# Kernel optimization log

Hardware: AMD Instinct MI355X
Metric: run time of the kernel (lower is better)

## Reference

```python
import jax, jax.numpy as jnp
import numpy as np

TEMPERATURE = 0.07
NEG = -1e9  # stand-in for -inf on the diagonal; exp(NEG) == 0


def setup_inputs() -> dict:
    key = jax.random.key(0)
    k1, k2, k3 = jax.random.split(key, 3)
    B, D = 4096, 1024
    return {
        "anchor_features": jax.random.normal(k1, (B, D), dtype=jnp.float32),
        "positive_features": jax.random.normal(k2, (B, D), dtype=jnp.float32),
        "labels": jax.random.randint(k3, (B,), 0, 2),
    }


def reference(anchor_features, positive_features, labels):
    B = anchor_features.shape[0]
    # L2-normalize (normalize=True)
    a = anchor_features / jnp.linalg.norm(anchor_features, axis=1, keepdims=True)
    p = positive_features / jnp.linalg.norm(positive_features, axis=1, keepdims=True)
    feats = jnp.concatenate([a, p], axis=0)                      # [2B, D]
    sim = jnp.matmul(feats, feats.T) / TEMPERATURE               # [2B, 2B]
    diag = jnp.eye(2 * B, dtype=bool)
    sim = jnp.where(diag, NEG, sim)                              # mask self-similarity
    # logsumexp over all non-self entries per row (diag contributes exp(NEG)=0)
    lse = jax.nn.logsumexp(sim, axis=1)                          # [2B]
    # positive pair similarity: sim[i, i+B] == sim[i+B, i] == <a_i, p_i>/t
    cross = jnp.sum(a * p, axis=1) / TEMPERATURE                 # [B]
    pos_sim = jnp.concatenate([cross, cross])                    # [2B]
    lab = jnp.concatenate([labels, labels]).astype(sim.dtype)    # [2B], 0/1
    per_row = (-pos_sim + lse) * lab
    num_pos = jnp.sum(lab)
    return jnp.where(num_pos > 0, jnp.sum(per_row) / num_pos, jnp.float32(0.0))
```

## Files before the change

### kernel.cpp

```cpp
#include <hip/hip_runtime.h>
#include <hip/hip_bf16.h>

#define TEMP_INV (1.0f / 0.07f)
#define LOG2E 1.4426950408889634f
#define LN2 0.6931471805599453f
#define CFIX 21.0f

typedef __attribute__((ext_vector_type(4))) float f32x4;

__device__ __forceinline__ void gload16(const unsigned char* g,
                                        unsigned char* l) {
  __builtin_amdgcn_global_load_lds(
      (const __attribute__((address_space(1))) void*)g,
      (__attribute__((address_space(3))) void*)l, 16, 0, 0);
}

__global__ __launch_bounds__(256) void norm_kernel(
    const float* __restrict__ A, const float* __restrict__ P,
    unsigned char* __restrict__ F, float* __restrict__ cross,
    float* __restrict__ lsum, int B, int D) {
  const int row = blockIdx.x;
  const int t = threadIdx.x;
  {
    const int zi = row * 256 + t;
    if (zi < 2 * B) lsum[zi] = 0.f;
  }
  const float4* a4 = reinterpret_cast<const float4*>(A + (size_t)row * D);
  const float4* p4 = reinterpret_cast<const float4*>(P + (size_t)row * D);
  const int n4 = D >> 2;
  float sa = 0.f, sp = 0.f, sx = 0.f;
  for (int i = t; i < n4; i += 256) {
    float4 av = a4[i], pv = p4[i];
    sa += av.x * av.x + av.y * av.y + av.z * av.z + av.w * av.w;
    sp += pv.x * pv.x + pv.y * pv.y + pv.z * pv.z + pv.w * pv.w;
    sx += av.x * pv.x + av.y * pv.y + av.z * pv.z + av.w * pv.w;
  }
#pragma unroll
  for (int off = 32; off; off >>= 1) {
    sa += __shfl_down(sa, off);
    sp += __shfl_down(sp, off);
    sx += __shfl_down(sx, off);
  }
  __shared__ float red[3][4];
  const int wid = t >> 6, lane = t & 63;
  if (lane == 0) { red[0][wid] = sa; red[1][wid] = sp; red[2][wid] = sx; }
  __syncthreads();
  sa = red[0][0] + red[0][1] + red[0][2] + red[0][3];
  sp = red[1][0] + red[1][1] + red[1][2] + red[1][3];
  sx = red[2][0] + red[2][1] + red[2][2] + red[2][3];
  const float ian = rsqrtf(sa), ipn = rsqrtf(sp);
  const float ia = ian * 16.f, ip = ipn * 16.f;
  unsigned char* fa = F + (size_t)row * D;
  unsigned char* fp = F + (size_t)(B + row) * D;
  for (int i = t; i < n4; i += 256) {
    float4 av = a4[i], pv = p4[i];
    int qa = 0, qp = 0;
    qa = __builtin_amdgcn_cvt_pk_fp8_f32(av.x * ia, av.y * ia, qa, false);
    qa = __builtin_amdgcn_cvt_pk_fp8_f32(av.z * ia, av.w * ia, qa, true);
    qp = __builtin_amdgcn_cvt_pk_fp8_f32(pv.x * ip, pv.y * ip, qp, false);
    qp = __builtin_amdgcn_cvt_pk_fp8_f32(pv.z * ip, pv.w * ip, qp, true);
    reinterpret_cast<int*>(fa)[i] = qa;
    reinterpret_cast<int*>(fp)[i] = qp;
  }
  if (t == 0) cross[row] = sx * ian * ipn;
}

#define VT 16

__global__ __launch_bounds__(512, 2) void gram_lse_kernel(
    const unsigned char* __restrict__ F, float* __restrict__ lsum, int NN,
    int D) {
  __shared__ unsigned char lds8[4][2][2][8192];
  const int nrb = NN >> 8;
  const int ntri = nrb * (nrb + 1) / 2;
  int b = blockIdx.x;
  b = (b & 7) * (gridDim.x >> 3) + (b >> 3);
  const int lin0 = b * 3;

  const int t = threadIdx.x;
  const int lane = t & 63, w = t >> 6;
  const int lo = lane & 15, hi = lane >> 4;
  const int wr = w >> 2, wn = w & 3;

  const int ci = t;
  const int lrS = ci >> 3, cuS = (ci & 7) ^ (lrS & 7);
  const int trowS = lrS * 4 + (cuS >> 1), kcS = (cuS & 1) << 4;
  const int dstW = w * 1024;

  int offA[8], offB[4];
#pragma unroll
  for (int mf = 0; mf < 8; ++mf) {
    const int r = wr * 128 + mf * 16 + lo;
    const int lr = r >> 2;
    const int cu = ((r & 3) << 1) | (hi >> 1);
    offA[mf] = lr * 128 + ((cu ^ (lr & 7)) << 4) + ((hi & 1) << 3);
  }
#pragma unroll
  for (int nf = 0; nf < 4; ++nf) {
    const int r = wn * 64 + nf * 16 + lo;
    const int lr = r >> 2;
    const int cu = ((r & 3) << 1) | (hi >> 1);
    offB[nf] = lr * 128 + ((cu ^ (lr & 7)) << 4) + ((hi & 1) << 3);
  }

  const float scl = LOG2E * TEMP_INV / 256.f;

  for (int ti = 0; ti < 3; ++ti) {
    const int lin = lin0 + ti;
    int by = (int)((sqrtf(8.f * (float)lin + 1.f) - 1.f) * 0.5f);
    while ((by + 1) * (by + 2) / 2 <= lin) ++by;
    while (by * (by + 1) / 2 > lin) --by;
    const int bx = lin - by * (by + 1) / 2;
    const int r0 = bx * 256;
    const int c0 = by * 256;
    const bool diag = (bx == by);

    const unsigned char* srcA = F + (size_t)(c0 + trowS) * D + kcS;
    const unsigned char* srcB = F + (size_t)(r0 + trowS) * D + kcS;

#define STAGE_A(T, KS)                                              \
  do {                                                              \
    int v_ = (T); if (v_ > VT - 1) v_ = VT - 1;                     \
    gload16(srcA + v_ * 64 + (KS) * 32, &lds8[(T) & 3][0][KS][dstW]); \
  } while (0)
#define STAGE_B(T, KS)                                              \
  do {                                                              \
    int v_ = (T); if (v_ > VT - 1) v_ = VT - 1;                     \
    gload16(srcB + v_ * 64 + (KS) * 32, &lds8[(T) & 3][1][KS][dstW]); \
  } while (0)

    f32x4 acc[8][4];
#pragma unroll
    for (int a = 0; a < 8; ++a)
#pragma unroll
      for (int bb = 0; bb < 4; ++bb) acc[a][bb] = (f32x4){0.f, 0.f, 0.f, 0.f};

#pragma unroll
    for (int pt = 0; pt < 3; ++pt) {
      STAGE_A(pt, 0); STAGE_B(pt, 0);
      STAGE_A(pt, 1); STAGE_B(pt, 1);
    }

    for (int v = 0; v < VT; ++v) {
      const int buf = v & 3;
      asm volatile("s_waitcnt vmcnt(8)" ::: "memory");
      __builtin_amdgcn_s_barrier();
      asm volatile("" ::: "memory");

#pragma unroll
      for (int KS = 0; KS < 2; ++KS) {
        const unsigned char* RA = &lds8[buf][0][KS][0];
        const unsigned char* RB = &lds8[buf][1][KS][0];
        long aF[8], bF[4];
#pragma unroll
        for (int nf = 0; nf < 4; ++nf) bF[nf] = *(const long*)(RB + offB[nf]);
#pragma unroll
        for (int mf = 0; mf < 8; ++mf) aF[mf] = *(const long*)(RA + offA[mf]);

        if (KS == 0) { STAGE_A(v + 3, 0); STAGE_B(v + 3, 0); }
        else         { STAGE_A(v + 3, 1); STAGE_B(v + 3, 1); }

        __builtin_amdgcn_s_setprio(1);
#pragma unroll
        for (int mf = 0; mf < 8; ++mf)
#pragma unroll
          for (int nf = 0; nf < 4; ++nf)
            acc[mf][nf] = __builtin_amdgcn_mfma_f32_16x16x32_fp8_fp8(
                aF[mf], bF[nf], acc[mf][nf], 0, 0, 0);
        __builtin_amdgcn_s_setprio(0);
      }
      asm volatile("" ::: "memory");
    }

    float s_i[4] = {0.f, 0.f, 0.f, 0.f};
    float s_j[32];
#pragma unroll
    for (int q = 0; q < 32; ++q) s_j[q] = 0.f;
    {
      const int jb2 = c0 + wr * 128;
#pragma unroll
      for (int nf = 0; nf < 4; ++nf) {
        const int dg = (r0 + wn * 64 + nf * 16 + lo) - jb2;
#pragma unroll
        for (int mf = 0; mf < 8; ++mf)
#pragma unroll
          for (int rg = 0; rg < 4; ++rg) {
            const int jloc = mf * 16 + hi * 4 + rg;
            float e = exp2f(acc[mf][nf][rg] * scl - CFIX);
            if (diag && dg == jloc) e = 0.f;
            s_i[nf] += e;
            s_j[mf * 4 + rg] += e;
          }
      }
    }
#pragma unroll
    for (int nf = 0; nf < 4; ++nf) {
      float v = s_i[nf];
      v += __shfl_xor(v, 16);
      v += __shfl_xor(v, 32);
      if (hi == 0) atomicAdd(&lsum[r0 + wn * 64 + nf * 16 + lo], v);
    }
    if (!diag) {
#pragma unroll
      for (int q = 0; q < 32; ++q) {
        float v = s_j[q];
        v += __shfl_xor(v, 1);
        v += __shfl_xor(v, 2);
        v += __shfl_xor(v, 4);
        v += __shfl_xor(v, 8);
        if (lo == 0)
          atomicAdd(&lsum[c0 + wr * 128 + (q >> 2) * 16 + hi * 4 + (q & 3)],
                    v);
      }
    }

    asm volatile("s_waitcnt vmcnt(0)" ::: "memory");
    __builtin_amdgcn_s_barrier();
    asm volatile("" ::: "memory");
#undef STAGE_A
#undef STAGE_B
  }
}

__global__ __launch_bounds__(256) void finalize_part(
    const float* __restrict__ lsum, const float* __restrict__ cross,
    const int* __restrict__ labels, float* __restrict__ bsum,
    float* __restrict__ bcnt, int B) {
  const int NN = 2 * B;
  const int i = blockIdx.x * 256 + threadIdx.x;
  float sum = 0.f, cnt = 0.f;
  if (i < NN) {
    const float lse = LN2 * (CFIX + log2f(lsum[i]));
    const float lab = (float)labels[i % B];
    sum = (lse - cross[i % B] * TEMP_INV) * lab;
    cnt = lab;
  }
#pragma unroll
  for (int off = 32; off; off >>= 1) {
    sum += __shfl_down(sum, off);
    cnt += __shfl_down(cnt, off);
  }
  __shared__ float rs[4], rc[4];
  const int wid = threadIdx.x >> 6, lane = threadIdx.x & 63;
  if (lane == 0) { rs[wid] = sum; rc[wid] = cnt; }
  __syncthreads();
  if (threadIdx.x == 0) {
    bsum[blockIdx.x] = rs[0] + rs[1] + rs[2] + rs[3];
    bcnt[blockIdx.x] = rc[0] + rc[1] + rc[2] + rc[3];
  }
}

__global__ __launch_bounds__(64) void finalize_final(
    const float* __restrict__ bsum, const float* __restrict__ bcnt,
    float* __restrict__ out, int nb) {
  const int t = threadIdx.x;
  float s = (t < nb) ? bsum[t] : 0.f;
  float c = (t < nb) ? bcnt[t] : 0.f;
#pragma unroll
  for (int off = 32; off; off >>= 1) {
    s += __shfl_down(s, off);
    c += __shfl_down(c, off);
  }
  if (t == 0) out[0] = (c > 0.f) ? s / c : 0.f;
}

extern "C" void kernel_launch(void* const* d_in, const int* in_sizes, int n_in,
                              void* d_out, int out_size, void* d_ws, size_t ws_size,
                              hipStream_t stream) {
  const float* A = (const float*)d_in[0];
  const float* P = (const float*)d_in[1];
  const int* labels = (const int*)d_in[2];
  float* out = (float*)d_out;
  const int B = in_sizes[2];
  const int D = in_sizes[0] / B;
  const int NN = 2 * B;

  char* ws = (char*)d_ws;
  unsigned char* F = (unsigned char*)ws;
  size_t off = (size_t)NN * D;
  off = (off + 255) & ~(size_t)255;
  float* cross = (float*)(ws + off);
  off += (size_t)B * sizeof(float);
  off = (off + 255) & ~(size_t)255;
  float* lsum = (float*)(ws + off);
  off += (size_t)NN * sizeof(float);
  off = (off + 255) & ~(size_t)255;
  float* bsum = (float*)(ws + off);
  off += 64 * sizeof(float);
  float* bcnt = (float*)(ws + off);

  norm_kernel<<<B, 256, 0, stream>>>(A, P, F, cross, lsum, B, D);
  const int nrb = NN >> 8;
  const int ntri = nrb * (nrb + 1) / 2;
  gram_lse_kernel<<<ntri / 3, 512, 0, stream>>>(F, lsum, NN, D);
  const int nb = (NN + 255) / 256;
  finalize_part<<<nb, 256, 0, stream>>>(lsum, cross, labels, bsum, bcnt, B);
  finalize_final<<<1, 64, 0, stream>>>(bsum, bcnt, out, nb);
}
```

Measured before the change: 115.4 us.

## Use 16x16x128 scaled FP8 MFMA with double-buffered 128-wide K staging, one tile per block

Replaces the 16x16x32 FP8 MFMA with the MX-scaled 16x16x128 f8f6f4 MFMA (unit scales), so each instruction covers four times the K depth. LDS staging changes from a 4-deep ring of 64-byte K slices to a 2-deep double buffer of 128-byte K slices, with a new swizzle and 128-bit LDS fragment reads. The grid now launches one block per triangle tile instead of each block looping over three tiles, which gives more blocks and less per-block serial work. The cost is a shallower pipeline that waits on vmcnt(0) every step, plus a higher register footprint for the 8-int fragments.

Measured after the change: 135.6 us. 17.6% more time.

```diff
diff --git a/kernel.cpp b/kernel.cpp
--- a/kernel.cpp
+++ b/kernel.cpp
@@ -7,6 +7,7 @@
 #define CFIX 21.0f
 
 typedef __attribute__((ext_vector_type(4))) float f32x4;
+typedef __attribute__((ext_vector_type(8))) int i32x8;
 
 __device__ __forceinline__ void gload16(const unsigned char* g,
                                         unsigned char* l) {
@@ -65,161 +66,147 @@
   if (t == 0) cross[row] = sx * ian * ipn;
 }
 
-#define VT 16
+#define UP 8
 
 __global__ __launch_bounds__(512, 2) void gram_lse_kernel(
     const unsigned char* __restrict__ F, float* __restrict__ lsum, int NN,
     int D) {
-  __shared__ unsigned char lds8[4][2][2][8192];
+  __shared__ unsigned char lds8[2][2][2][16384];
   const int nrb = NN >> 8;
   const int ntri = nrb * (nrb + 1) / 2;
-  int b = blockIdx.x;
-  b = (b & 7) * (gridDim.x >> 3) + (b >> 3);
-  const int lin0 = b * 3;
+  int lin = blockIdx.x;
+  lin = (lin & 7) * (ntri >> 3) + (lin >> 3);
+  int by = (int)((sqrtf(8.f * (float)lin + 1.f) - 1.f) * 0.5f);
+  while ((by + 1) * (by + 2) / 2 <= lin) ++by;
+  while (by * (by + 1) / 2 > lin) --by;
+  const int bx = lin - by * (by + 1) / 2;
+  const int r0 = bx * 256;
+  const int c0 = by * 256;
+  const bool diag = (bx == by);
 
   const int t = threadIdx.x;
   const int lane = t & 63, w = t >> 6;
   const int lo = lane & 15, hi = lane >> 4;
   const int wr = w >> 2, wn = w & 3;
 
-  const int ci = t;
-  const int lrS = ci >> 3, cuS = (ci & 7) ^ (lrS & 7);
-  const int trowS = lrS * 4 + (cuS >> 1), kcS = (cuS & 1) << 4;
-  const int dstW = w * 1024;
-
-  int offA[8], offB[4];
-#pragma unroll
-  for (int mf = 0; mf < 8; ++mf) {
-    const int r = wr * 128 + mf * 16 + lo;
-    const int lr = r >> 2;
-    const int cu = ((r & 3) << 1) | (hi >> 1);
-    offA[mf] = lr * 128 + ((cu ^ (lr & 7)) << 4) + ((hi & 1) << 3);
-  }
-#pragma unroll
-  for (int nf = 0; nf < 4; ++nf) {
-    const int r = wn * 64 + nf * 16 + lo;
-    const int lr = r >> 2;
-    const int cu = ((r & 3) << 1) | (hi >> 1);
-    offB[nf] = lr * 128 + ((cu ^ (lr & 7)) << 4) + ((hi & 1) << 3);
-  }
-
-  const float scl = LOG2E * TEMP_INV / 256.f;
-
-  for (int ti = 0; ti < 3; ++ti) {
-    const int lin = lin0 + ti;
-    int by = (int)((sqrtf(8.f * (float)lin + 1.f) - 1.f) * 0.5f);
-    while ((by + 1) * (by + 2) / 2 <= lin) ++by;
-    while (by * (by + 1) / 2 > lin) --by;
-    const int bx = lin - by * (by + 1) / 2;
-    const int r0 = bx * 256;
-    const int c0 = by * 256;
-    const bool diag = (bx == by);
-
-    const unsigned char* srcA = F + (size_t)(c0 + trowS) * D + kcS;
-    const unsigned char* srcB = F + (size_t)(r0 + trowS) * D + kcS;
-
-#define STAGE_A(T, KS)                                              \
-  do {                                                              \
-    int v_ = (T); if (v_ > VT - 1) v_ = VT - 1;                     \
-    gload16(srcA + v_ * 64 + (KS) * 32, &lds8[(T) & 3][0][KS][dstW]); \
+  const int l0_ = t >> 3, c0_ = (t & 7) ^ (l0_ & 7);
+  const int rS0 = (l0_ << 1) | (c0_ >> 2), kS0 = c0_ & 3;
+  const int t1 = t + 512;
+  const int l1_ = t1 >> 3, c1_ = (t1 & 7) ^ (l1_ & 7);
+  const int rS1 = (l1_ << 1) | (c1_ >> 2), kS1 = c1_ & 3;
+  const unsigned char* sA0 = F + (size_t)(c0 + rS0) * D + kS0 * 16;
+  const unsigned char* sA1 = F + (size_t)(c0 + rS1) * D + kS1 * 16;
+  const unsigned char* sB0 = F + (size_t)(r0 + rS0) * D + kS0 * 16;
+  const unsigned char* sB1 = F + (size_t)(r0 + rS1) * D + kS1 * 16;
+  const int dst0 = w * 1024;
+  const int dst1 = 8192 + w * 1024;
+
+  const int p0 = (((lo & 1) << 2) | ((hi & 1) << 1)) ^ ((lo >> 1) & 7);
+  const int rdA = (hi >> 1) * 16384 + wr * 8192 + (lo >> 1) * 128 + p0 * 16;
+  const int rdA2 = rdA ^ 16;
+  const int rdB = (hi >> 1) * 16384 + wn * 4096 + (lo >> 1) * 128 + p0 * 16;
+  const int rdB2 = rdB ^ 16;
+
+#define STAGE_PAIR(U, PB)                                            \
+  do {                                                               \
+    const int o0 = (2 * (U)) * 64, o1 = o0 + 64;                     \
+    gload16(sA0 + o0, &lds8[PB][0][0][dst0]);                        \
+    gload16(sA1 + o0, &lds8[PB][0][0][dst1]);                        \
+    gload16(sA0 + o1, &lds8[PB][0][1][dst0]);                        \
+    gload16(sA1 + o1, &lds8[PB][0][1][dst1]);                        \
+    gload16(sB0 + o0, &lds8[PB][1][0][dst0]);                        \
+    gload16(sB1 + o0, &lds8[PB][1][0][dst1]);                        \
+    gload16(sB0 + o1, &lds8[PB][1][1][dst0]);                        \
+    gload16(sB1 + o1, &lds8[PB][1][1][dst1]);                        \
   } while (0)
-#define STAGE_B(T, KS)                                              \
-  do {                                                              \
-    int v_ = (T); if (v_ > VT - 1) v_ = VT - 1;                     \
-    gload16(srcB + v_ * 64 + (KS) * 32, &lds8[(T) & 3][1][KS][dstW]); \
-  } while (0)
-
-    f32x4 acc[8][4];
-#pragma unroll
-    for (int a = 0; a < 8; ++a)
-#pragma unroll
-      for (int bb = 0; bb < 4; ++bb) acc[a][bb] = (f32x4){0.f, 0.f, 0.f, 0.f};
-
-#pragma unroll
-    for (int pt = 0; pt < 3; ++pt) {
-      STAGE_A(pt, 0); STAGE_B(pt, 0);
-      STAGE_A(pt, 1); STAGE_B(pt, 1);
-    }
-
-    for (int v = 0; v < VT; ++v) {
-      const int buf = v & 3;
-      asm volatile("s_waitcnt vmcnt(8)" ::: "memory");
-      __builtin_amdgcn_s_barrier();
-      asm volatile("" ::: "memory");
-
-#pragma unroll
-      for (int KS = 0; KS < 2; ++KS) {
-        const unsigned char* RA = &lds8[buf][0][KS][0];
-        const unsigned char* RB = &lds8[buf][1][KS][0];
-        long aF[8], bF[4];
-#pragma unroll
-        for (int nf = 0; nf < 4; ++nf) bF[nf] = *(const long*)(RB + offB[nf]);
-#pragma unroll
-        for (int mf = 0; mf < 8; ++mf) aF[mf] = *(const long*)(RA + offA[mf]);
-
-        if (KS == 0) { STAGE_A(v + 3, 0); STAGE_B(v + 3, 0); }
-        else         { STAGE_A(v + 3, 1); STAGE_B(v + 3, 1); }
-
-        __builtin_amdgcn_s_setprio(1);
-#pragma unroll
-        for (int mf = 0; mf < 8; ++mf)
-#pragma unroll
-          for (int nf = 0; nf < 4; ++nf)
-            acc[mf][nf] = __builtin_amdgcn_mfma_f32_16x16x32_fp8_fp8(
-                aF[mf], bF[nf], acc[mf][nf], 0, 0, 0);
-        __builtin_amdgcn_s_setprio(0);
-      }
-      asm volatile("" ::: "memory");
-    }
-
-    float s_i[4] = {0.f, 0.f, 0.f, 0.f};
-    float s_j[32];
-#pragma unroll
-    for (int q = 0; q < 32; ++q) s_j[q] = 0.f;
-    {
-      const int jb2 = c0 + wr * 128;
-#pragma unroll
-      for (int nf = 0; nf < 4; ++nf) {
-        const int dg = (r0 + wn * 64 + nf * 16 + lo) - jb2;
-#pragma unroll
-        for (int mf = 0; mf < 8; ++mf)
-#pragma unroll
-          for (int rg = 0; rg < 4; ++rg) {
-            const int jloc = mf * 16 + hi * 4 + rg;
-            float e = exp2f(acc[mf][nf][rg] * scl - CFIX);
-            if (diag && dg == jloc) e = 0.f;
-            s_i[nf] += e;
-            s_j[mf * 4 + rg] += e;
-          }
-      }
-    }
-#pragma unroll
-    for (int nf = 0; nf < 4; ++nf) {
-      float v = s_i[nf];
-      v += __shfl_xor(v, 16);
-      v += __shfl_xor(v, 32);
-      if (hi == 0) atomicAdd(&lsum[r0 + wn * 64 + nf * 16 + lo], v);
-    }
-    if (!diag) {
-#pragma unroll
-      for (int q = 0; q < 32; ++q) {
-        float v = s_j[q];
-        v += __shfl_xor(v, 1);
-        v += __shfl_xor(v, 2);
-        v += __shfl_xor(v, 4);
-        v += __shfl_xor(v, 8);
-        if (lo == 0)
-          atomicAdd(&lsum[c0 + wr * 128 + (q >> 2) * 16 + hi * 4 + (q & 3)],
-                    v);
-      }
-    }
-
+
+  f32x4 acc[8][4];
+#pragma unroll
+  for (int a = 0; a < 8; ++a)
+#pragma unroll
+    for (int bb = 0; bb < 4; ++bb) acc[a][bb] = (f32x4){0.f, 0.f, 0.f, 0.f};
+
+  STAGE_PAIR(0, 0);
+
+  for (int u = 0; u < UP; ++u) {
+    const int pr = u & 1;
     asm volatile("s_waitcnt vmcnt(0)" ::: "memory");
     __builtin_amdgcn_s_barrier();
     asm volatile("" ::: "memory");
-#undef STAGE_A
-#undef STAGE_B
-  }
+
+    const unsigned char* RA = &lds8[pr][0][0][0];
+    const unsigned char* RB = &lds8[pr][1][0][0];
+    i32x8 bfr[4];
+#pragma unroll
+    for (int nf = 0; nf < 4; ++nf) {
+      int4 q0 = *(const int4*)(RB + rdB + nf * 1024);
+      int4 q1 = *(const int4*)(RB + rdB2 + nf * 1024);
+      bfr[nf][0] = q0.x; bfr[nf][1] = q0.y; bfr[nf][2] = q0.z;
+      bfr[nf][3] = q0.w; bfr[nf][4] = q1.x; bfr[nf][5] = q1.y;
+      bfr[nf][6] = q1.z; bfr[nf][7] = q1.w;
+    }
+
+    if (u + 1 < UP) STAGE_PAIR(u + 1, pr ^ 1);
+
+    __builtin_amdgcn_s_setprio(1);
+#pragma unroll
+    for (int mf = 0; mf < 8; ++mf) {
+      int4 q0 = *(const int4*)(RA + rdA + mf * 1024);
+      int4 q1 = *(const int4*)(RA + rdA2 + mf * 1024);
+      i32x8 af;
+      af[0] = q0.x; af[1] = q0.y; af[2] = q0.z; af[3] = q0.w;
+      af[4] = q1.x; af[5] = q1.y; af[6] = q1.z; af[7] = q1.w;
+#pragma unroll
+      for (int nf = 0; nf < 4; ++nf)
+        acc[mf][nf] = __builtin_amdgcn_mfma_scale_f32_16x16x128_f8f6f4(
+            af, bfr[nf], acc[mf][nf], 0, 0, 0, 127, 0, 127);
+    }
+    __builtin_amdgcn_s_setprio(0);
+    asm volatile("" ::: "memory");
+  }
+
+  const float scl = LOG2E * TEMP_INV / 256.f;
+  float s_i[4] = {0.f, 0.f, 0.f, 0.f};
+  float s_j[32];
+#pragma unroll
+  for (int q = 0; q < 32; ++q) s_j[q] = 0.f;
+  {
+    const int jb2 = c0 + wr * 128;
+#pragma unroll
+    for (int nf = 0; nf < 4; ++nf) {
+      const int dg = (r0 + wn * 64 + nf * 16 + lo) - jb2;
+#pragma unroll
+      for (int mf = 0; mf < 8; ++mf)
+#pragma unroll
+        for (int rg = 0; rg < 4; ++rg) {
+          const int jloc = mf * 16 + hi * 4 + rg;
+          float e = exp2f(acc[mf][nf][rg] * scl - CFIX);
+          if (diag && dg == jloc) e = 0.f;
+          s_i[nf] += e;
+          s_j[mf * 4 + rg] += e;
+        }
+    }
+  }
+#pragma unroll
+  for (int nf = 0; nf < 4; ++nf) {
+    float v = s_i[nf];
+    v += __shfl_xor(v, 16);
+    v += __shfl_xor(v, 32);
+    if (hi == 0) atomicAdd(&lsum[r0 + wn * 64 + nf * 16 + lo], v);
+  }
+  if (!diag) {
+#pragma unroll
+    for (int q = 0; q < 32; ++q) {
+      float v = s_j[q];
+      v += __shfl_xor(v, 1);
+      v += __shfl_xor(v, 2);
+      v += __shfl_xor(v, 4);
+      v += __shfl_xor(v, 8);
+      if (lo == 0)
+        atomicAdd(&lsum[c0 + wr * 128 + (q >> 2) * 16 + hi * 4 + (q & 3)], v);
+    }
+  }
+#undef STAGE_PAIR
 }
 
 __global__ __launch_bounds__(256) void finalize_part(
@@ -292,7 +279,7 @@
   norm_kernel<<<B, 256, 0, stream>>>(A, P, F, cross, lsum, B, D);
   const int nrb = NN >> 8;
   const int ntri = nrb * (nrb + 1) / 2;
-  gram_lse_kernel<<<ntri / 3, 512, 0, stream>>>(F, lsum, NN, D);
+  gram_lse_kernel<<<ntri, 512, 0, stream>>>(F, lsum, NN, D);
   const int nb = (NN + 255) / 256;
   finalize_part<<<nb, 256, 0, stream>>>(lsum, cross, labels, bsum, bcnt, B);
   finalize_final<<<1, 64, 0, stream>>>(bsum, bcnt, out, nb);
```

## Launch one block per triangular tile and split tail tiles into halves

Applied to the files above, without the earlier changes.

The Gram/LSE kernel previously launched ntri/3 blocks that each looped over three upper-triangular tiles. It now launches one block per tile and splits the last 16 tiles into two 128-column half tiles, using a templated body with MFN=4 for the halves. This is meant to fill many more CUs and shrink the tail imbalance. The K-step loop is also merged so both LDS fragment sets are read before the MFMAs. The cost is a larger grid, redundant A loads in the half tiles, and more atomics on lsum.

New measurement: 116.1 us. Within noise of the previous version (+0.6%).

```diff
diff --git a/kernel.cpp b/kernel.cpp
--- a/kernel.cpp
+++ b/kernel.cpp
@@ -65,7 +65,145 @@
   if (t == 0) cross[row] = sx * ian * ipn;
 }
 
-#define VT 16
+template <int MFN>
+__device__ __forceinline__ void gram_body(
+    unsigned char* LDS, const unsigned char* F, float* lsum, int D,
+    int r0, int c0, bool diag) {
+  const int t = threadIdx.x;
+  const int lane = t & 63, w = t >> 6;
+  const int lo = lane & 15, hi = lane >> 4;
+  const int wr = w >> 2, wn = w & 3;
+
+  const int ciA = t & (MFN * 64 - 1);
+  const int lrA = ciA >> 3, cuA = (ciA & 7) ^ (lrA & 7);
+  const int trA = lrA * 4 + (cuA >> 1), kcA = (cuA & 1) << 4;
+  const int lrB = t >> 3, cuB = (t & 7) ^ (lrB & 7);
+  const int trB = lrB * 4 + (cuB >> 1), kcB = (cuB & 1) << 4;
+  const unsigned char* sA = F + (size_t)(c0 + trA) * D + kcA;
+  const unsigned char* sB = F + (size_t)(r0 + trB) * D + kcB;
+  const int dstA = (w % MFN) * 1024;
+  const int dstB = w * 1024;
+
+  int offA[MFN], offB[4];
+#pragma unroll
+  for (int mf = 0; mf < MFN; ++mf) {
+    const int r = wr * (MFN * 16) + mf * 16 + lo;
+    const int lr = r >> 2;
+    const int cu = ((r & 3) << 1) | (hi >> 1);
+    offA[mf] = lr * 128 + ((cu ^ (lr & 7)) << 4) + ((hi & 1) << 3);
+  }
+#pragma unroll
+  for (int nf = 0; nf < 4; ++nf) {
+    const int r = wn * 64 + nf * 16 + lo;
+    const int lr = r >> 2;
+    const int cu = ((r & 3) << 1) | (hi >> 1);
+    offB[nf] = lr * 128 + ((cu ^ (lr & 7)) << 4) + ((hi & 1) << 3);
+  }
+
+#define STAGE(V, KS)                                                       \
+  do {                                                                    \
+    int v_ = (V); if (v_ > 15) v_ = 15;                                   \
+    const int o_ = v_ * 64 + (KS) * 32;                                   \
+    gload16(sA + o_, LDS + ((V) & 3) * 32768 + (KS) * 8192 + dstA);       \
+    gload16(sB + o_, LDS + ((V) & 3) * 32768 + 16384 + (KS) * 8192 + dstB); \
+  } while (0)
+
+  f32x4 acc[MFN][4];
+#pragma unroll
+  for (int a = 0; a < MFN; ++a)
+#pragma unroll
+    for (int bb = 0; bb < 4; ++bb) acc[a][bb] = (f32x4){0.f, 0.f, 0.f, 0.f};
+
+  STAGE(0, 0); STAGE(0, 1);
+  STAGE(1, 0); STAGE(1, 1);
+  STAGE(2, 0); STAGE(2, 1);
+
+  for (int v = 0; v < 16; ++v) {
+    const int buf = v & 3;
+    asm volatile("s_waitcnt vmcnt(8)" ::: "memory");
+    __builtin_amdgcn_s_barrier();
+    asm volatile("" ::: "memory");
+
+    const unsigned char* RA0 = LDS + buf * 32768;
+    const unsigned char* RA1 = RA0 + 8192;
+    const unsigned char* RB0 = LDS + buf * 32768 + 16384;
+    const unsigned char* RB1 = RB0 + 8192;
+    long a0[MFN], a1[MFN], b0[4], b1[4];
+#pragma unroll
+    for (int nf = 0; nf < 4; ++nf) b0[nf] = *(const long*)(RB0 + offB[nf]);
+#pragma unroll
+    for (int mf = 0; mf < MFN; ++mf) a0[mf] = *(const long*)(RA0 + offA[mf]);
+#pragma unroll
+    for (int nf = 0; nf < 4; ++nf) b1[nf] = *(const long*)(RB1 + offB[nf]);
+#pragma unroll
+    for (int mf = 0; mf < MFN; ++mf) a1[mf] = *(const long*)(RA1 + offA[mf]);
+
+    STAGE(v + 3, 0);
+    STAGE(v + 3, 1);
+
+    __builtin_amdgcn_s_setprio(1);
+#pragma unroll
+    for (int mf = 0; mf < MFN; ++mf)
+#pragma unroll
+      for (int nf = 0; nf < 4; ++nf)
+        acc[mf][nf] = __builtin_amdgcn_mfma_f32_16x16x32_fp8_fp8(
+            a0[mf], b0[nf], acc[mf][nf], 0, 0, 0);
+#pragma unroll
+    for (int mf = 0; mf < MFN; ++mf)
+#pragma unroll
+      for (int nf = 0; nf < 4; ++nf)
+        acc[mf][nf] = __builtin_amdgcn_mfma_f32_16x16x32_fp8_fp8(
+            a1[mf], b1[nf], acc[mf][nf], 0, 0, 0);
+    __builtin_amdgcn_s_setprio(0);
+    asm volatile("" ::: "memory");
+  }
+
+  const float scl = LOG2E * TEMP_INV / 256.f;
+  float s_i[4] = {0.f, 0.f, 0.f, 0.f};
+  float s_j[MFN * 4];
+#pragma unroll
+  for (int q = 0; q < MFN * 4; ++q) s_j[q] = 0.f;
+  {
+    const int jb2 = c0 + wr * (MFN * 16);
+#pragma unroll
+    for (int nf = 0; nf < 4; ++nf) {
+      const int dg = (r0 + wn * 64 + nf * 16 + lo) - jb2;
+#pragma unroll
+      for (int mf = 0; mf < MFN; ++mf)
+#pragma unroll
+        for (int rg = 0; rg < 4; ++rg) {
+          const int jloc = mf * 16 + hi * 4 + rg;
+          float e = exp2f(acc[mf][nf][rg] * scl - CFIX);
+          if (diag && dg == jloc) e = 0.f;
+          s_i[nf] += e;
+          s_j[mf * 4 + rg] += e;
+        }
+    }
+  }
+#pragma unroll
+  for (int nf = 0; nf < 4; ++nf) {
+    float v = s_i[nf];
+    v += __shfl_xor(v, 16);
+    v += __shfl_xor(v, 32);
+    if (hi == 0) atomicAdd(&lsum[r0 + wn * 64 + nf * 16 + lo], v);
+  }
+  if (!diag) {
+#pragma unroll
+    for (int q = 0; q < MFN * 4; ++q) {
+      float v = s_j[q];
+      v += __shfl_xor(v, 1);
+      v += __shfl_xor(v, 2);
+      v += __shfl_xor(v, 4);
+      v += __shfl_xor(v, 8);
+      if (lo == 0)
+        atomicAdd(&lsum[c0 + wr * (MFN * 16) + (q >> 2) * 16 + hi * 4 +
+                        (q & 3)],
+                  v);
+    }
+  }
+  asm volatile("s_waitcnt vmcnt(0)" ::: "memory");
+#undef STAGE
+}
 
 __global__ __launch_bounds__(512, 2) void gram_lse_kernel(
     const unsigned char* __restrict__ F, float* __restrict__ lsum, int NN,
@@ -73,153 +211,31 @@
   __shared__ unsigned char lds8[4][2][2][8192];
   const int nrb = NN >> 8;
   const int ntri = nrb * (nrb + 1) / 2;
-  int b = blockIdx.x;
-  b = (b & 7) * (gridDim.x >> 3) + (b >> 3);
-  const int lin0 = b * 3;
-
-  const int t = threadIdx.x;
-  const int lane = t & 63, w = t >> 6;
-  const int lo = lane & 15, hi = lane >> 4;
-  const int wr = w >> 2, wn = w & 3;
-
-  const int ci = t;
-  const int lrS = ci >> 3, cuS = (ci & 7) ^ (lrS & 7);
-  const int trowS = lrS * 4 + (cuS >> 1), kcS = (cuS & 1) << 4;
-  const int dstW = w * 1024;
-
-  int offA[8], offB[4];
-#pragma unroll
-  for (int mf = 0; mf < 8; ++mf) {
-    const int r = wr * 128 + mf * 16 + lo;
-    const int lr = r >> 2;
-    const int cu = ((r & 3) << 1) | (hi >> 1);
-    offA[mf] = lr * 128 + ((cu ^ (lr & 7)) << 4) + ((hi & 1) << 3);
-  }
-#pragma unroll
-  for (int nf = 0; nf < 4; ++nf) {
-    const int r = wn * 64 + nf * 16 + lo;
-    const int lr = r >> 2;
-    const int cu = ((r & 3) << 1) | (hi >> 1);
-    offB[nf] = lr * 128 + ((cu ^ (lr & 7)) << 4) + ((hi & 1) << 3);
-  }
-
-  const float scl = LOG2E * TEMP_INV / 256.f;
-
-  for (int ti = 0; ti < 3; ++ti) {
-    const int lin = lin0 + ti;
-    int by = (int)((sqrtf(8.f * (float)lin + 1.f) - 1.f) * 0.5f);
-    while ((by + 1) * (by + 2) / 2 <= lin) ++by;
-    while (by * (by + 1) / 2 > lin) --by;
-    const int bx = lin - by * (by + 1) / 2;
-    const int r0 = bx * 256;
-    const int c0 = by * 256;
-    const bool diag = (bx == by);
-
-    const unsigned char* srcA = F + (size_t)(c0 + trowS) * D + kcS;
-    const unsigned char* srcB = F + (size_t)(r0 + trowS) * D + kcS;
-
-#define STAGE_A(T, KS)                                              \
-  do {                                                              \
-    int v_ = (T); if (v_ > VT - 1) v_ = VT - 1;                     \
-    gload16(srcA + v_ * 64 + (KS) * 32, &lds8[(T) & 3][0][KS][dstW]); \
-  } while (0)
-#define STAGE_B(T, KS)                                              \
-  do {                                                              \
-    int v_ = (T); if (v_ > VT - 1) v_ = VT - 1;                     \
-    gload16(srcB + v_ * 64 + (KS) * 32, &lds8[(T) & 3][1][KS][dstW]); \
-  } while (0)
-
-    f32x4 acc[8][4];
-#pragma unroll
-    for (int a = 0; a < 8; ++a)
-#pragma unroll
-      for (int bb = 0; bb < 4; ++bb) acc[a][bb] = (f32x4){0.f, 0.f, 0.f, 0.f};
-
-#pragma unroll
-    for (int pt = 0; pt < 3; ++pt) {
-      STAGE_A(pt, 0); STAGE_B(pt, 0);
-      STAGE_A(pt, 1); STAGE_B(pt, 1);
-    }
-
-    for (int v = 0; v < VT; ++v) {
-      const int buf = v & 3;
-      asm volatile("s_waitcnt vmcnt(8)" ::: "memory");
-      __builtin_amdgcn_s_barrier();
-      asm volatile("" ::: "memory");
-
-#pragma unroll
-      for (int KS = 0; KS < 2; ++KS) {
-        const unsigned char* RA = &lds8[buf][0][KS][0];
-        const unsigned char* RB = &lds8[buf][1][KS][0];
-        long aF[8], bF[4];
-#pragma unroll
-        for (int nf = 0; nf < 4; ++nf) bF[nf] = *(const long*)(RB + offB[nf]);
-#pragma unroll
-        for (int mf = 0; mf < 8; ++mf) aF[mf] = *(const long*)(RA + offA[mf]);
-
-        if (KS == 0) { STAGE_A(v + 3, 0); STAGE_B(v + 3, 0); }
-        else         { STAGE_A(v + 3, 1); STAGE_B(v + 3, 1); }
-
-        __builtin_amdgcn_s_setprio(1);
-#pragma unroll
-        for (int mf = 0; mf < 8; ++mf)
-#pragma unroll
-          for (int nf = 0; nf < 4; ++nf)
-            acc[mf][nf] = __builtin_amdgcn_mfma_f32_16x16x32_fp8_fp8(
-                aF[mf], bF[nf], acc[mf][nf], 0, 0, 0);
-        __builtin_amdgcn_s_setprio(0);
-      }
-      asm volatile("" ::: "memory");
-    }
-
-    float s_i[4] = {0.f, 0.f, 0.f, 0.f};
-    float s_j[32];
-#pragma unroll
-    for (int q = 0; q < 32; ++q) s_j[q] = 0.f;
-    {
-      const int jb2 = c0 + wr * 128;
-#pragma unroll
-      for (int nf = 0; nf < 4; ++nf) {
-        const int dg = (r0 + wn * 64 + nf * 16 + lo) - jb2;
-#pragma unroll
-        for (int mf = 0; mf < 8; ++mf)
-#pragma unroll
-          for (int rg = 0; rg < 4; ++rg) {
-            const int jloc = mf * 16 + hi * 4 + rg;
-            float e = exp2f(acc[mf][nf][rg] * scl - CFIX);
-            if (diag && dg == jloc) e = 0.f;
-            s_i[nf] += e;
-            s_j[mf * 4 + rg] += e;
-          }
-      }
-    }
-#pragma unroll
-    for (int nf = 0; nf < 4; ++nf) {
-      float v = s_i[nf];
-      v += __shfl_xor(v, 16);
-      v += __shfl_xor(v, 32);
-      if (hi == 0) atomicAdd(&lsum[r0 + wn * 64 + nf * 16 + lo], v);
-    }
-    if (!diag) {
-#pragma unroll
-      for (int q = 0; q < 32; ++q) {
-        float v = s_j[q];
-        v += __shfl_xor(v, 1);
-        v += __shfl_xor(v, 2);
-        v += __shfl_xor(v, 4);
-        v += __shfl_xor(v, 8);
-        if (lo == 0)
-          atomicAdd(&lsum[c0 + wr * 128 + (q >> 2) * 16 + hi * 4 + (q & 3)],
-                    v);
-      }
-    }
-
-    asm volatile("s_waitcnt vmcnt(0)" ::: "memory");
-    __builtin_amdgcn_s_barrier();
-    asm volatile("" ::: "memory");
-#undef STAGE_A
-#undef STAGE_B
-  }
+  const int nfull = ntri - 16;
+  const int bidx = blockIdx.x;
+  int lin, c0extra = 0;
+  bool half = false;
+  if (bidx < nfull) {
+    lin = bidx;
+    if ((nfull & 7) == 0) lin = (bidx & 7) * (nfull >> 3) + (bidx >> 3);
+  } else {
+    const int idx = bidx - nfull;
+    lin = nfull + (idx >> 1);
+    c0extra = (idx & 1) * 128;
+    half = true;
+  }
+  int by = (int)((sqrtf(8.f * (float)lin + 1.f) - 1.f) * 0.5f);
+  while ((by + 1) * (by + 2) / 2 <= lin) ++by;
+  while (by * (by + 1) / 2 > lin) --by;
+  const int bx = lin - by * (by + 1) / 2;
+  const int r0 = bx * 256;
+  const int c0 = by * 256 + c0extra;
+  const bool diag = (bx == by);
+
+  if (!half)
+    gram_body<8>(&lds8[0][0][0][0], F, lsum, D, r0, c0, diag);
+  else
+    gram_body<4>(&lds8[0][0][0][0], F, lsum, D, r0, c0, diag);
 }
 
 __global__ __launch_bounds__(256) void finalize_part(
@@ -292,7 +308,8 @@
   norm_kernel<<<B, 256, 0, stream>>>(A, P, F, cross, lsum, B, D);
   const int nrb = NN >> 8;
   const int ntri = nrb * (nrb + 1) / 2;
-  gram_lse_kernel<<<ntri / 3, 512, 0, stream>>>(F, lsum, NN, D);
+  const int nblk = (ntri - 16) + 32;
+  gram_lse_kernel<<<nblk, 512, 0, stream>>>(F, lsum, NN, D);
   const int nb = (NN + 255) / 256;
   finalize_part<<<nb, 256, 0, stream>>>(lsum, cross, labels, bsum, bcnt, B);
   finalize_final<<<1, 64, 0, stream>>>(bsum, bcnt, out, nb);
```

## Split Gram tiles across 16-wave blocks and launch one block per tile

Applied to the files above, without the earlier changes.

The fused Gram/logsumexp kernel is restructured so each 256x256 triangular tile is handled by a 1024-thread block. Each wave now owns a 64x64 sub-tile, and the two K-substeps are staged by separate wave halves. The grid grows from 176 blocks that each loop over three tiles to 512 blocks, with the first 16 taking one extra tile. The aim is to fill all compute units instead of leaving many idle. In exchange, per-wave register reuse is lower and the grid size and tile count are hardcoded for NN=8192.

Result: no change. 115.7 us (+0.2%).

```diff
diff --git a/kernel.cpp b/kernel.cpp
--- a/kernel.cpp
+++ b/kernel.cpp
@@ -65,32 +65,28 @@
   if (t == 0) cross[row] = sx * ian * ipn;
 }
 
-#define VT 16
-
-__global__ __launch_bounds__(512, 2) void gram_lse_kernel(
-    const unsigned char* __restrict__ F, float* __restrict__ lsum, int NN,
-    int D) {
-  __shared__ unsigned char lds8[4][2][2][8192];
-  const int nrb = NN >> 8;
-  const int ntri = nrb * (nrb + 1) / 2;
-  int b = blockIdx.x;
-  b = (b & 7) * (gridDim.x >> 3) + (b >> 3);
-  const int lin0 = b * 3;
-
+
+__device__ __forceinline__ void gram_tile(
+    unsigned char* LDS8, const unsigned char* F, float* lsum, int D,
+    int r0, int c0, bool diag) {
   const int t = threadIdx.x;
   const int lane = t & 63, w = t >> 6;
   const int lo = lane & 15, hi = lane >> 4;
   const int wr = w >> 2, wn = w & 3;
 
-  const int ci = t;
-  const int lrS = ci >> 3, cuS = (ci & 7) ^ (lrS & 7);
-  const int trowS = lrS * 4 + (cuS >> 1), kcS = (cuS & 1) << 4;
-  const int dstW = w * 1024;
-
-  int offA[8], offB[4];
-#pragma unroll
-  for (int mf = 0; mf < 8; ++mf) {
-    const int r = wr * 128 + mf * 16 + lo;
+  const int KSa = t >> 9;
+  const int cS = t & 511;
+  const int lineS = cS >> 3, pS = (cS & 7) ^ (lineS & 7);
+  const int trS = lineS * 4 + (pS >> 1);
+  const int kcS = ((pS & 1) << 4) + KSa * 32;
+  const unsigned char* sA = F + (size_t)(c0 + trS) * D + kcS;
+  const unsigned char* sB = F + (size_t)(r0 + trS) * D + kcS;
+  const int dstW = (w & 7) * 1024;
+
+  int offA[4], offB[4];
+#pragma unroll
+  for (int mf = 0; mf < 4; ++mf) {
+    const int r = wr * 64 + mf * 16 + lo;
     const int lr = r >> 2;
     const int cu = ((r & 3) << 1) | (hi >> 1);
     offA[mf] = lr * 128 + ((cu ^ (lr & 7)) << 4) + ((hi & 1) << 3);
@@ -103,10 +99,119 @@
     offB[nf] = lr * 128 + ((cu ^ (lr & 7)) << 4) + ((hi & 1) << 3);
   }
 
+#define STAGE(V)                                                        \
+  do {                                                                  \
+    int v_ = (V); if (v_ > 15) v_ = 15;                                 \
+    gload16(sA + v_ * 64,                                               \
+            LDS8 + ((V) & 3) * 32768 + KSa * 8192 + dstW);              \
+    gload16(sB + v_ * 64,                                               \
+            LDS8 + ((V) & 3) * 32768 + 16384 + KSa * 8192 + dstW);      \
+  } while (0)
+
+  f32x4 acc[4][4];
+#pragma unroll
+  for (int a = 0; a < 4; ++a)
+#pragma unroll
+    for (int bb = 0; bb < 4; ++bb) acc[a][bb] = (f32x4){0.f, 0.f, 0.f, 0.f};
+
+  STAGE(0); STAGE(1); STAGE(2);
+
+  for (int v = 0; v < 16; ++v) {
+    const int buf = v & 3;
+    asm volatile("s_waitcnt vmcnt(4)" ::: "memory");
+    __builtin_amdgcn_s_barrier();
+    asm volatile("" ::: "memory");
+
+    long a0[4], a1[4], b0[4], b1[4];
+#pragma unroll
+    for (int q = 0; q < 4; ++q) {
+      b0[q] = *(const long*)(LDS8 + buf * 32768 + 16384 + offB[q]);
+      a0[q] = *(const long*)(LDS8 + buf * 32768 + offA[q]);
+      b1[q] = *(const long*)(LDS8 + buf * 32768 + 16384 + 8192 + offB[q]);
+      a1[q] = *(const long*)(LDS8 + buf * 32768 + 8192 + offA[q]);
+    }
+
+    STAGE(v + 3);
+
+    __builtin_amdgcn_s_setprio(1);
+#pragma unroll
+    for (int mf = 0; mf < 4; ++mf)
+#pragma unroll
+      for (int nf = 0; nf < 4; ++nf)
+        acc[mf][nf] = __builtin_amdgcn_mfma_f32_16x16x32_fp8_fp8(
+            a0[mf], b0[nf], acc[mf][nf], 0, 0, 0);
+#pragma unroll
+    for (int mf = 0; mf < 4; ++mf)
+#pragma unroll
+      for (int nf = 0; nf < 4; ++nf)
+        acc[mf][nf] = __builtin_amdgcn_mfma_f32_16x16x32_fp8_fp8(
+            a1[mf], b1[nf], acc[mf][nf], 0, 0, 0);
+    __builtin_amdgcn_s_setprio(0);
+    asm volatile("" ::: "memory");
+  }
+
   const float scl = LOG2E * TEMP_INV / 256.f;
-
-  for (int ti = 0; ti < 3; ++ti) {
-    const int lin = lin0 + ti;
+  float s_i[4] = {0.f, 0.f, 0.f, 0.f};
+  float s_j[16];
+#pragma unroll
+  for (int q = 0; q < 16; ++q) s_j[q] = 0.f;
+  {
+    const int dgb = (r0 + wn * 64) - (c0 + wr * 64);
+#pragma unroll
+    for (int nf = 0; nf < 4; ++nf) {
+      const int dg = dgb + nf * 16 + lo;
+#pragma unroll
+      for (int mf = 0; mf < 4; ++mf)
+#pragma unroll
+        for (int rg = 0; rg < 4; ++rg) {
+          const int jloc = mf * 16 + hi * 4 + rg;
+          float e = exp2f(acc[mf][nf][rg] * scl - CFIX);
+          if (diag && dg == jloc) e = 0.f;
+          s_i[nf] += e;
+          s_j[mf * 4 + rg] += e;
+        }
+    }
+  }
+#pragma unroll
+  for (int nf = 0; nf < 4; ++nf) {
+    float v = s_i[nf];
+    v += __shfl_xor(v, 16);
+    v += __shfl_xor(v, 32);
+    if (hi == 0) atomicAdd(&lsum[r0 + wn * 64 + nf * 16 + lo], v);
+  }
+  if (!diag) {
+#pragma unroll
+    for (int q = 0; q < 16; ++q) {
+      float v = s_j[q];
+      v += __shfl_xor(v, 1);
+      v += __shfl_xor(v, 2);
+      v += __shfl_xor(v, 4);
+      v += __shfl_xor(v, 8);
+      if (lo == 0)
+        atomicAdd(&lsum[c0 + wr * 64 + (q >> 2) * 16 + hi * 4 + (q & 3)], v);
+    }
+  }
+  asm volatile("s_waitcnt vmcnt(0)" ::: "memory");
+  __builtin_amdgcn_s_barrier();
+  asm volatile("" ::: "memory");
+#undef STAGE
+}
+
+__global__ __launch_bounds__(1024) void gram_full_kernel(
+    const unsigned char* __restrict__ F, float* __restrict__ lsum, int NN,
+    int D) {
+  __shared__ unsigned char lds8[4][2][2][8192];
+  const int bid = blockIdx.x;
+  const int nT = (bid < 16) ? 2 : 1;
+
+  for (int ti = 0; ti < nT; ++ti) {
+    int lin;
+    if (ti == 0) {
+      lin = bid;
+      lin = (lin & 7) * 64 + (lin >> 3);
+    } else {
+      lin = 512 + bid;
+    }
     int by = (int)((sqrtf(8.f * (float)lin + 1.f) - 1.f) * 0.5f);
     while ((by + 1) * (by + 2) / 2 <= lin) ++by;
     while (by * (by + 1) / 2 > lin) --by;
@@ -114,111 +219,7 @@
     const int r0 = bx * 256;
     const int c0 = by * 256;
     const bool diag = (bx == by);
-
-    const unsigned char* srcA = F + (size_t)(c0 + trowS) * D + kcS;
-    const unsigned char* srcB = F + (size_t)(r0 + trowS) * D + kcS;
-
-#define STAGE_A(T, KS)                                              \
-  do {                                                              \
-    int v_ = (T); if (v_ > VT - 1) v_ = VT - 1;                     \
-    gload16(srcA + v_ * 64 + (KS) * 32, &lds8[(T) & 3][0][KS][dstW]); \
-  } while (0)
-#define STAGE_B(T, KS)                                              \
-  do {                                                              \
-    int v_ = (T); if (v_ > VT - 1) v_ = VT - 1;                     \
-    gload16(srcB + v_ * 64 + (KS) * 32, &lds8[(T) & 3][1][KS][dstW]); \
-  } while (0)
-
-    f32x4 acc[8][4];
-#pragma unroll
-    for (int a = 0; a < 8; ++a)
-#pragma unroll
-      for (int bb = 0; bb < 4; ++bb) acc[a][bb] = (f32x4){0.f, 0.f, 0.f, 0.f};
-
-#pragma unroll
-    for (int pt = 0; pt < 3; ++pt) {
-      STAGE_A(pt, 0); STAGE_B(pt, 0);
-      STAGE_A(pt, 1); STAGE_B(pt, 1);
-    }
-
-    for (int v = 0; v < VT; ++v) {
-      const int buf = v & 3;
-      asm volatile("s_waitcnt vmcnt(8)" ::: "memory");
-      __builtin_amdgcn_s_barrier();
-      asm volatile("" ::: "memory");
-
-#pragma unroll
-      for (int KS = 0; KS < 2; ++KS) {
-        const unsigned char* RA = &lds8[buf][0][KS][0];
-        const unsigned char* RB = &lds8[buf][1][KS][0];
-        long aF[8], bF[4];
-#pragma unroll
-        for (int nf = 0; nf < 4; ++nf) bF[nf] = *(const long*)(RB + offB[nf]);
-#pragma unroll
-        for (int mf = 0; mf < 8; ++mf) aF[mf] = *(const long*)(RA + offA[mf]);
-
-        if (KS == 0) { STAGE_A(v + 3, 0); STAGE_B(v + 3, 0); }
-        else         { STAGE_A(v + 3, 1); STAGE_B(v + 3, 1); }
-
-        __builtin_amdgcn_s_setprio(1);
-#pragma unroll
-        for (int mf = 0; mf < 8; ++mf)
-#pragma unroll
-          for (int nf = 0; nf < 4; ++nf)
-            acc[mf][nf] = __builtin_amdgcn_mfma_f32_16x16x32_fp8_fp8(
-                aF[mf], bF[nf], acc[mf][nf], 0, 0, 0);
-        __builtin_amdgcn_s_setprio(0);
-      }
-      asm volatile("" ::: "memory");
-    }
-
-    float s_i[4] = {0.f, 0.f, 0.f, 0.f};
-    float s_j[32];
-#pragma unroll
-    for (int q = 0; q < 32; ++q) s_j[q] = 0.f;
-    {
-      const int jb2 = c0 + wr * 128;
-#pragma unroll
-      for (int nf = 0; nf < 4; ++nf) {
-        const int dg = (r0 + wn * 64 + nf * 16 + lo) - jb2;
-#pragma unroll
-        for (int mf = 0; mf < 8; ++mf)
-#pragma unroll
-          for (int rg = 0; rg < 4; ++rg) {
-            const int jloc = mf * 16 + hi * 4 + rg;
-            float e = exp2f(acc[mf][nf][rg] * scl - CFIX);
-            if (diag && dg == jloc) e = 0.f;
-            s_i[nf] += e;
-            s_j[mf * 4 + rg] += e;
-          }
-      }
-    }
-#pragma unroll
-    for (int nf = 0; nf < 4; ++nf) {
-      float v = s_i[nf];
-      v += __shfl_xor(v, 16);
-      v += __shfl_xor(v, 32);
-      if (hi == 0) atomicAdd(&lsum[r0 + wn * 64 + nf * 16 + lo], v);
-    }
-    if (!diag) {
-#pragma unroll
-      for (int q = 0; q < 32; ++q) {
-        float v = s_j[q];
-        v += __shfl_xor(v, 1);
-        v += __shfl_xor(v, 2);
-        v += __shfl_xor(v, 4);
-        v += __shfl_xor(v, 8);
-        if (lo == 0)
-          atomicAdd(&lsum[c0 + wr * 128 + (q >> 2) * 16 + hi * 4 + (q & 3)],
-                    v);
-      }
-    }
-
-    asm volatile("s_waitcnt vmcnt(0)" ::: "memory");
-    __builtin_amdgcn_s_barrier();
-    asm volatile("" ::: "memory");
-#undef STAGE_A
-#undef STAGE_B
+    gram_tile(&lds8[0][0][0][0], F, lsum, D, r0, c0, diag);
   }
 }
 
@@ -290,9 +291,7 @@
   float* bcnt = (float*)(ws + off);
 
   norm_kernel<<<B, 256, 0, stream>>>(A, P, F, cross, lsum, B, D);
-  const int nrb = NN >> 8;
-  const int ntri = nrb * (nrb + 1) / 2;
-  gram_lse_kernel<<<ntri / 3, 512, 0, stream>>>(F, lsum, NN, D);
+  gram_full_kernel<<<512, 1024, 0, stream>>>(F, lsum, NN, D);
   const int nb = (NN + 255) / 256;
   finalize_part<<<nb, 256, 0, stream>>>(lsum, cross, labels, bsum, bcnt, B);
   finalize_final<<<1, 64, 0, stream>>>(bsum, bcnt, out, nb);
```
